# Kernel tuning notes

Hardware: AMD Instinct MI355X
Metric: run time of the kernel (lower is better)

## Reference

```python
import jax, jax.numpy as jnp
import numpy as np

BASE_TEMP = 0.07
CLASS_TEMPS = jnp.array([0.08, 0.05, 0.10], dtype=jnp.float32)  # idx 0,1,2
EPS = 1e-08


def setup_inputs() -> dict:
    key = jax.random.key(0)
    k1, k2 = jax.random.split(key)
    B, D = 8192, 128
    embeddings = jax.random.normal(k1, (B, D), dtype=jnp.float32)
    labels = jax.random.randint(k2, (B,), 0, 3, dtype=jnp.int64)
    return {"embeddings": embeddings, "labels": labels}


def reference(embeddings, labels):
    B = embeddings.shape[0]
    # per-row temperature from the row's class label
    temps = CLASS_TEMPS[labels]  # [B]
    sim = jnp.matmul(embeddings, embeddings.T)  # [B, B]
    logits = sim / temps[:, None]
    # subtract detached row max (stability, gradient-stopped as in .detach())
    logits = logits - jax.lax.stop_gradient(jnp.max(logits, axis=1, keepdims=True))
    # denominator includes the self term (original sums exp over all j)
    log_prob = logits - jnp.log(jnp.sum(jnp.exp(logits), axis=1, keepdims=True) + EPS)
    # positives: same label, excluding self
    pos_mask = (labels[:, None] == labels[None, :]).astype(jnp.float32)
    pos_mask = pos_mask * (1.0 - jnp.eye(B, dtype=jnp.float32))
    pos_count = jnp.sum(pos_mask, axis=1)  # [B]
    valid = pos_count > 0
    loss_i = -(BASE_TEMP / temps) * jnp.sum(pos_mask * log_prob, axis=1) / (pos_count + EPS)
    n_valid = jnp.sum(valid.astype(jnp.float32))
    total = jnp.sum(jnp.where(valid, loss_i, 0.0))
    return jnp.where(n_valid > 0, total / jnp.maximum(n_valid, 1.0), 0.0)
```

## Files before the change

kernel.cpp:

```cpp
#include <hip/hip_runtime.h>
#include <hip/hip_bf16.h>


#define B_ROWS 8192
#define D_DIM 128
#define BASE_TEMP 0.07f
#define LOG2E 1.4426950408889634f
#define LN2 0.6931471805599453f
#define FIX_SCALE 1048576.0f

typedef __bf16 bf16x8 __attribute__((ext_vector_type(8)));
typedef __bf16 bf16x4 __attribute__((ext_vector_type(4)));
typedef float floatx16 __attribute__((ext_vector_type(16)));
typedef unsigned long long u64;

__device__ __forceinline__ float class_invtemp(int lbl) {
    return (lbl == 0) ? 12.5f : ((lbl == 1) ? 20.0f : 10.0f);
}

__device__ __forceinline__ u64 fix64(float v) {
    return (u64)(long long)llrintf(v * FIX_SCALE);
}

__global__ __launch_bounds__(256) void kz_zero(u64* __restrict__ a) {
    a[threadIdx.x] = 0ull;
    a[256 + threadIdx.x] = 0ull;
}

__global__ __launch_bounds__(256) void k0_prep(
        const float* __restrict__ E, const int* __restrict__ labels,
        __bf16* __restrict__ Ebf, float* __restrict__ nrm,
        u64* __restrict__ Sfix , u64* __restrict__ cntfix ) {
    const int blk = blockIdx.x;
    const int tid = threadIdx.x;
    const int row0 = blk * 32;

    __shared__ float sh[3][128];
    __shared__ int scnt[3];
    if (tid < 3) scnt[tid] = 0;

    const float4* src = reinterpret_cast<const float4*>(E + (size_t)row0 * D_DIM);
    #pragma unroll
    for (int p = 0; p < 4; ++p) {
        int idx = p * 256 + tid;
        float4 v = src[idx];
        int r = idx >> 5, k4 = idx & 31;
        int R = row0 + r;
        int T = R >> 5;
        int l = (R & 31) + ((k4 >> 1) & 1) * 32;
        int c = k4 >> 2;
        size_t dst = (size_t)T * 4096 + c * 512 + l * 8 + (k4 & 1) * 4;
        bf16x4 o = { (__bf16)v.x, (__bf16)v.y, (__bf16)v.z, (__bf16)v.w };
        *reinterpret_cast<bf16x4*>(Ebf + dst) = o;
        float s = v.x * v.x + v.y * v.y + v.z * v.z + v.w * v.w;
        s += __shfl_xor(s, 1);  s += __shfl_xor(s, 2);  s += __shfl_xor(s, 4);
        s += __shfl_xor(s, 8);  s += __shfl_xor(s, 16);
        if ((tid & 31) == 0) nrm[R] = s;
    }

    const int d = tid & 127, half = tid >> 7;
    float s0 = 0.f, s1 = 0.f, s2 = 0.f;
    #pragma unroll 4
    for (int r2 = 0; r2 < 16; ++r2) {
        int r = row0 + half * 16 + r2;
        float v = E[(size_t)r * D_DIM + d];
        int l = labels[r];
        s0 += (l == 0) ? v : 0.f;
        s1 += (l == 1) ? v : 0.f;
        s2 += (l == 2) ? v : 0.f;
    }
    if (half == 1) { sh[0][d] = s0; sh[1][d] = s1; sh[2][d] = s2; }
    __syncthreads();
    if (half == 0) {
        atomicAdd(&Sfix[d],       fix64(s0 + sh[0][d]));
        atomicAdd(&Sfix[128 + d], fix64(s1 + sh[1][d]));
        atomicAdd(&Sfix[256 + d], fix64(s2 + sh[2][d]));
    }
    if (tid < 32) atomicAdd(&scnt[labels[row0 + tid]], 1);
    __syncthreads();
    if (tid < 3) atomicAdd(&cntfix[tid], (u64)scnt[tid]);
}

__global__ __launch_bounds__(256, 3) void k2_stats(
        const __bf16* __restrict__ Ebf, const int* __restrict__ labels,
        const float* __restrict__ nrm, float* __restrict__ part,
        int nsplit, int jrange) {
    const int lane = threadIdx.x & 63;
    const int wave = threadIdx.x >> 6;
    const int split = blockIdx.y;
    const int j0 = split * jrange;
    const int col = lane & 31;
    const int icol = blockIdx.x * 128 + wave * 32 + col;

    const float bscale = class_invtemp(labels[icol]) * LOG2E;
    const float negm = -bscale * nrm[icol];

    const int iT = blockIdx.x * 4 + wave;
    const __bf16* bbase = Ebf + (size_t)iT * 4096 + lane * 8;
    bf16x8 Bf[8];
    #pragma unroll
    for (int c = 0; c < 8; ++c) {
        bf16x8 raw = *reinterpret_cast<const bf16x8*>(bbase + c * 512);
        bf16x8 sc;
        #pragma unroll
        for (int e = 0; e < 8; ++e) sc[e] = (__bf16)((float)raw[e] * bscale);
        Bf[c] = sc;
    }

    const __bf16* abase = Ebf + ((size_t)(j0 >> 5)) * 4096 + lane * 8;
    bf16x8 A0[8], A1[8];
    #pragma unroll
    for (int c = 0; c < 8; ++c)
        A0[c] = *reinterpret_cast<const bf16x8*>(abase + c * 512);

    float Zacc[16];
    #pragma unroll
    for (int r = 0; r < 16; ++r) Zacc[r] = 0.f;
    const int nsteps = jrange >> 5;

    auto k2_step = [&](const bf16x8* Ab) {
        floatx16 acc;
        #pragma unroll
        for (int r = 0; r < 16; ++r) acc[r] = negm;
        #pragma unroll
        for (int c = 0; c < 8; ++c)
            acc = __builtin_amdgcn_mfma_f32_32x32x16_bf16(Ab[c], Bf[c], acc, 0, 0, 0);
        #pragma unroll
        for (int r = 0; r < 16; ++r)
            Zacc[r] += __builtin_amdgcn_exp2f(acc[r]);
    };

    for (int s = 0; s < nsteps; s += 2) {
        {
            const __bf16* ap = abase + (size_t)(s + 1) * 4096;
            #pragma unroll
            for (int c = 0; c < 8; ++c)
                A1[c] = *reinterpret_cast<const bf16x8*>(ap + c * 512);
            k2_step(A0);
        }
        {
            if (s + 2 < nsteps) {
                const __bf16* ap = abase + (size_t)(s + 2) * 4096;
                #pragma unroll
                for (int c = 0; c < 8; ++c)
                    A0[c] = *reinterpret_cast<const bf16x8*>(ap + c * 512);
            }
            k2_step(A1);
        }
    }

    float t0 = (Zacc[0] + Zacc[1]) + (Zacc[2] + Zacc[3]);
    float t1 = (Zacc[4] + Zacc[5]) + (Zacc[6] + Zacc[7]);
    float t2 = (Zacc[8] + Zacc[9]) + (Zacc[10] + Zacc[11]);
    float t3 = (Zacc[12] + Zacc[13]) + (Zacc[14] + Zacc[15]);
    float Zt = (t0 + t1) + (t2 + t3);
    Zt += __shfl_xor(Zt, 32);
    if (lane < 32)
        part[(size_t)split * B_ROWS + icol] = Zt;
}

__global__ __launch_bounds__(256) void k3_rowloss(
        const float* __restrict__ E, const int* __restrict__ labels,
        const u64* __restrict__ Sfix, const u64* __restrict__ cntfix,
        const float* __restrict__ nrm, const float* __restrict__ part,
        int nsplit, u64* __restrict__ lossfix, u64* __restrict__ validfix,
        unsigned int* __restrict__ done, float* __restrict__ out) {
    __shared__ float sS[384];
    const int tid = threadIdx.x;
    if (tid < 128) {
        sS[tid]       = (float)(long long)Sfix[tid]       * (1.0f / FIX_SCALE);
        sS[128 + tid] = (float)(long long)Sfix[128 + tid] * (1.0f / FIX_SCALE);
        sS[256 + tid] = (float)(long long)Sfix[256 + tid] * (1.0f / FIX_SCALE);
    }
    __syncthreads();

    const int r = tid >> 3, g = tid & 7;
    const int i = blockIdx.x * 32 + r;
    const int lab = labels[i];
    const float invt = class_invtemp(lab);

    const float4* er = reinterpret_cast<const float4*>(E + (size_t)i * D_DIM);
    const float4* sr = reinterpret_cast<const float4*>(&sS[lab * 128]);
    float dotS = 0.f;
    #pragma unroll
    for (int q = 0; q < 4; ++q) {
        float4 v = er[g * 4 + q];
        float4 s = sr[g * 4 + q];
        dotS += v.x * s.x + v.y * s.y + v.z * s.z + v.w * s.w;
    }
    float Zp = 0.f;
    for (int p = g; p < nsplit; p += 8)
        Zp += part[(size_t)p * B_ROWS + i];

    #pragma unroll
    for (int off = 1; off < 8; off <<= 1) {
        dotS += __shfl_xor(dotS, off);
        Zp   += __shfl_xor(Zp, off);
    }

    float loss = 0.f;
    int valid = 0;
    if (g == 0) {
        const float nr = nrm[i];
        const float C = (float)(long long)cntfix[lab] - 1.0f;
        const float lse = invt * nr + LN2 * __builtin_amdgcn_logf(Zp);
        const float P_nat = invt * (dotS - nr);
        if (C > 0.f) {
            loss = -(BASE_TEMP * invt) * (P_nat - C * lse) / (C + 1e-8f);
            valid = 1;
        }
    }
    loss  += __shfl_down(loss, 8);   valid += __shfl_down(valid, 8);
    loss  += __shfl_down(loss, 16);  valid += __shfl_down(valid, 16);
    loss  += __shfl_down(loss, 32);  valid += __shfl_down(valid, 32);

    __shared__ float rl[4];
    __shared__ int rv[4];
    if ((tid & 63) == 0) { rl[tid >> 6] = loss; rv[tid >> 6] = valid; }
    __syncthreads();
    if (tid == 0) {
        float bt = (rl[0] + rl[1]) + (rl[2] + rl[3]);
        int bv = (rv[0] + rv[1]) + (rv[2] + rv[3]);
        atomicAdd(lossfix, fix64(bt));
        atomicAdd(validfix, (u64)bv);
        __threadfence();
        unsigned int t = atomicAdd(done, 1u);
        if (t == gridDim.x - 1) {
            u64 L = atomicAdd(lossfix, 0ull);
            u64 V = atomicAdd(validfix, 0ull);
            double T = (double)(long long)L * (1.0 / (double)FIX_SCALE);
            double N = (double)(long long)V;
            out[0] = (N > 0.0) ? (float)(T / fmax(N, 1.0)) : 0.f;
        }
    }
}

extern "C" void kernel_launch(void* const* d_in, const int* in_sizes, int n_in,
                              void* d_out, int out_size, void* d_ws, size_t ws_size,
                              hipStream_t stream) {
    const float* E = (const float*)d_in[0];
    const int* labels = (const int*)d_in[1];
    float* out = (float*)d_out;
    char* ws = (char*)d_ws;

    const size_t OFF_EBF = 0;
    const size_t OFF_ATOM = (size_t)2 << 20;
    const size_t OFF_NRM = OFF_ATOM + 4096;
    const size_t OFF_PART = OFF_NRM + (size_t)B_ROWS * 4;

    int nsplit = 8;
    if (ws_size >= OFF_PART + (size_t)32 * B_ROWS * 4) nsplit = 32;
    else if (ws_size >= OFF_PART + (size_t)16 * B_ROWS * 4) nsplit = 16;
    const int jrange = B_ROWS / nsplit;

    __bf16* Ebf = (__bf16*)(ws + OFF_EBF);
    u64* Sfix = (u64*)(ws + OFF_ATOM);
    u64* cntfix = Sfix + 384;
    u64* lossfix = Sfix + 388;
    u64* validfix = Sfix + 389;
    unsigned int* done = (unsigned int*)(Sfix + 390);
    float* nrm = (float*)(ws + OFF_NRM);
    float* part = (float*)(ws + OFF_PART);

    kz_zero<<<1, 256, 0, stream>>>(Sfix);
    k0_prep<<<256, 256, 0, stream>>>(E, labels, Ebf, nrm, Sfix, cntfix);
    k2_stats<<<dim3(64, nsplit), 256, 0, stream>>>(Ebf, labels, nrm, part, nsplit, jrange);
    k3_rowloss<<<256, 256, 0, stream>>>(E, labels, Sfix, cntfix, nrm, part,
                                        nsplit, lossfix, validfix, done, out);
}
```

Baseline: 55.57 us.

## Fuse all stages into one cooperative persistent kernel with grid syncs

Replaces the four separate launches (zero, prep, stats, rowloss) with a single cooperative kernel that separates the phases with grid-wide syncs. Fixed-point atomics are replaced by per-block partial buffers that are reduced deterministically. The prep stage now also writes a pre-scaled bf16 copy, so the MFMA stage no longer rescales B. The MFMA chain is split into two independent accumulators to expose instruction-level parallelism. In exchange it pays grid-sync costs and may get lower occupancy from the larger fused kernel.

```diff
diff --git a/kernel.cpp b/kernel.cpp
--- a/kernel.cpp
+++ b/kernel.cpp
@@ -1,236 +1,259 @@
 #include <hip/hip_runtime.h>
 #include <hip/hip_bf16.h>
+#include <hip/hip_cooperative_groups.h>
+
+namespace cg = cooperative_groups;
 
 
 #define B_ROWS 8192
 #define D_DIM 128
+#define NSPLIT 32
+#define JRANGE (B_ROWS / NSPLIT)
+#define NSTEPS (JRANGE / 32)
+#define NUNITS (64 * NSPLIT)
 #define BASE_TEMP 0.07f
 #define LOG2E 1.4426950408889634f
 #define LN2 0.6931471805599453f
-#define FIX_SCALE 1048576.0f
 
 typedef __bf16 bf16x8 __attribute__((ext_vector_type(8)));
 typedef __bf16 bf16x4 __attribute__((ext_vector_type(4)));
 typedef float floatx16 __attribute__((ext_vector_type(16)));
-typedef unsigned long long u64;
 
 __device__ __forceinline__ float class_invtemp(int lbl) {
     return (lbl == 0) ? 12.5f : ((lbl == 1) ? 20.0f : 10.0f);
 }
 
-__device__ __forceinline__ u64 fix64(float v) {
-    return (u64)(long long)llrintf(v * FIX_SCALE);
-}
-
-__global__ __launch_bounds__(256) void kz_zero(u64* __restrict__ a) {
-    a[threadIdx.x] = 0ull;
-    a[256 + threadIdx.x] = 0ull;
-}
-
-__global__ __launch_bounds__(256) void k0_prep(
+__global__ __launch_bounds__(256, 3) void supcon_all(
         const float* __restrict__ E, const int* __restrict__ labels,
-        __bf16* __restrict__ Ebf, float* __restrict__ nrm,
-        u64* __restrict__ Sfix , u64* __restrict__ cntfix ) {
-    const int blk = blockIdx.x;
+        __bf16* __restrict__ Ebf, __bf16* __restrict__ Ebs,
+        float* __restrict__ nrm,
+        float* __restrict__ Spart ,
+        int* __restrict__ cntpart ,
+        float* __restrict__ S , float* __restrict__ counts ,
+        float* __restrict__ part ,
+        float* __restrict__ bpart , float* __restrict__ out) {
+    cg::grid_group gg = cg::this_grid();
     const int tid = threadIdx.x;
-    const int row0 = blk * 32;
+    const int bid = blockIdx.x;
+    const int nblk = gridDim.x;
 
     __shared__ float sh[3][128];
     __shared__ int scnt[3];
-    if (tid < 3) scnt[tid] = 0;
-
-    const float4* src = reinterpret_cast<const float4*>(E + (size_t)row0 * D_DIM);
-    #pragma unroll
-    for (int p = 0; p < 4; ++p) {
-        int idx = p * 256 + tid;
-        float4 v = src[idx];
-        int r = idx >> 5, k4 = idx & 31;
-        int R = row0 + r;
-        int T = R >> 5;
-        int l = (R & 31) + ((k4 >> 1) & 1) * 32;
-        int c = k4 >> 2;
-        size_t dst = (size_t)T * 4096 + c * 512 + l * 8 + (k4 & 1) * 4;
-        bf16x4 o = { (__bf16)v.x, (__bf16)v.y, (__bf16)v.z, (__bf16)v.w };
-        *reinterpret_cast<bf16x4*>(Ebf + dst) = o;
-        float s = v.x * v.x + v.y * v.y + v.z * v.z + v.w * v.w;
-        s += __shfl_xor(s, 1);  s += __shfl_xor(s, 2);  s += __shfl_xor(s, 4);
-        s += __shfl_xor(s, 8);  s += __shfl_xor(s, 16);
-        if ((tid & 31) == 0) nrm[R] = s;
-    }
-
-    const int d = tid & 127, half = tid >> 7;
-    float s0 = 0.f, s1 = 0.f, s2 = 0.f;
-    #pragma unroll 4
-    for (int r2 = 0; r2 < 16; ++r2) {
-        int r = row0 + half * 16 + r2;
-        float v = E[(size_t)r * D_DIM + d];
-        int l = labels[r];
-        s0 += (l == 0) ? v : 0.f;
-        s1 += (l == 1) ? v : 0.f;
-        s2 += (l == 2) ? v : 0.f;
-    }
-    if (half == 1) { sh[0][d] = s0; sh[1][d] = s1; sh[2][d] = s2; }
-    __syncthreads();
-    if (half == 0) {
-        atomicAdd(&Sfix[d],       fix64(s0 + sh[0][d]));
-        atomicAdd(&Sfix[128 + d], fix64(s1 + sh[1][d]));
-        atomicAdd(&Sfix[256 + d], fix64(s2 + sh[2][d]));
-    }
-    if (tid < 32) atomicAdd(&scnt[labels[row0 + tid]], 1);
-    __syncthreads();
-    if (tid < 3) atomicAdd(&cntfix[tid], (u64)scnt[tid]);
-}
-
-__global__ __launch_bounds__(256, 3) void k2_stats(
-        const __bf16* __restrict__ Ebf, const int* __restrict__ labels,
-        const float* __restrict__ nrm, float* __restrict__ part,
-        int nsplit, int jrange) {
-    const int lane = threadIdx.x & 63;
-    const int wave = threadIdx.x >> 6;
-    const int split = blockIdx.y;
-    const int j0 = split * jrange;
-    const int col = lane & 31;
-    const int icol = blockIdx.x * 128 + wave * 32 + col;
-
-    const float bscale = class_invtemp(labels[icol]) * LOG2E;
-    const float negm = -bscale * nrm[icol];
-
-    const int iT = blockIdx.x * 4 + wave;
-    const __bf16* bbase = Ebf + (size_t)iT * 4096 + lane * 8;
-    bf16x8 Bf[8];
-    #pragma unroll
-    for (int c = 0; c < 8; ++c) {
-        bf16x8 raw = *reinterpret_cast<const bf16x8*>(bbase + c * 512);
-        bf16x8 sc;
-        #pragma unroll
-        for (int e = 0; e < 8; ++e) sc[e] = (__bf16)((float)raw[e] * bscale);
-        Bf[c] = sc;
-    }
-
-    const __bf16* abase = Ebf + ((size_t)(j0 >> 5)) * 4096 + lane * 8;
-    bf16x8 A0[8], A1[8];
-    #pragma unroll
-    for (int c = 0; c < 8; ++c)
-        A0[c] = *reinterpret_cast<const bf16x8*>(abase + c * 512);
-
-    float Zacc[16];
-    #pragma unroll
-    for (int r = 0; r < 16; ++r) Zacc[r] = 0.f;
-    const int nsteps = jrange >> 5;
-
-    auto k2_step = [&](const bf16x8* Ab) {
-        floatx16 acc;
-        #pragma unroll
-        for (int r = 0; r < 16; ++r) acc[r] = negm;
+    __shared__ float rl[4];
+    __shared__ int rv[4];
+
+    for (int g = bid; g < 256; g += nblk) {
+        const int row0 = g * 32;
+        if (tid < 3) scnt[tid] = 0;
+        __syncthreads();
+        const float4* src = reinterpret_cast<const float4*>(E + (size_t)row0 * D_DIM);
+        #pragma unroll
+        for (int p = 0; p < 4; ++p) {
+            int idx = p * 256 + tid;
+            float4 v = src[idx];
+            int r = idx >> 5, k4 = idx & 31;
+            int R = row0 + r;
+            float sc = class_invtemp(labels[R]) * LOG2E;
+            int T = R >> 5;
+            int l = (R & 31) + ((k4 >> 1) & 1) * 32;
+            int c = k4 >> 2;
+            size_t dst = (size_t)T * 4096 + c * 512 + l * 8 + (k4 & 1) * 4;
+            bf16x4 o  = { (__bf16)v.x, (__bf16)v.y, (__bf16)v.z, (__bf16)v.w };
+            bf16x4 os = { (__bf16)(v.x * sc), (__bf16)(v.y * sc),
+                          (__bf16)(v.z * sc), (__bf16)(v.w * sc) };
+            *reinterpret_cast<bf16x4*>(Ebf + dst) = o;
+            *reinterpret_cast<bf16x4*>(Ebs + dst) = os;
+            float s = v.x * v.x + v.y * v.y + v.z * v.z + v.w * v.w;
+            s += __shfl_xor(s, 1);  s += __shfl_xor(s, 2);  s += __shfl_xor(s, 4);
+            s += __shfl_xor(s, 8);  s += __shfl_xor(s, 16);
+            if ((tid & 31) == 0) nrm[R] = s;
+        }
+        const int d = tid & 127, half = tid >> 7;
+        float s0 = 0.f, s1 = 0.f, s2 = 0.f;
+        #pragma unroll 4
+        for (int r2 = 0; r2 < 16; ++r2) {
+            int r = row0 + half * 16 + r2;
+            float v = E[(size_t)r * D_DIM + d];
+            int l = labels[r];
+            s0 += (l == 0) ? v : 0.f;
+            s1 += (l == 1) ? v : 0.f;
+            s2 += (l == 2) ? v : 0.f;
+        }
+        if (half == 1) { sh[0][d] = s0; sh[1][d] = s1; sh[2][d] = s2; }
+        if (tid < 32) atomicAdd(&scnt[labels[row0 + tid]], 1);
+        __syncthreads();
+        if (half == 0) {
+            Spart[((size_t)g * 3 + 0) * 128 + d] = s0 + sh[0][d];
+            Spart[((size_t)g * 3 + 1) * 128 + d] = s1 + sh[1][d];
+            Spart[((size_t)g * 3 + 2) * 128 + d] = s2 + sh[2][d];
+        }
+        if (tid < 3) cntpart[g * 4 + tid] = scnt[tid];
+        __syncthreads();
+    }
+    gg.sync();
+
+    if (bid < 3) {
+        if (tid < 128) {
+            float a = 0.f;
+            #pragma unroll 8
+            for (int g = 0; g < 256; ++g)
+                a += Spart[((size_t)g * 3 + bid) * 128 + tid];
+            S[bid * 128 + tid] = a;
+        }
+    } else if (bid == 3 && tid < 3) {
+        int a = 0;
+        #pragma unroll 8
+        for (int g = 0; g < 256; ++g) a += cntpart[g * 4 + tid];
+        counts[tid] = (float)a;
+    }
+
+    for (int u = bid; u < NUNITS; u += nblk) {
+        const int itile = u >> 5;
+        const int split = u & 31;
+        const int j0 = split * JRANGE;
+        const int lane = tid & 63;
+        const int wave = tid >> 6;
+        const int col = lane & 31;
+        const int icol = itile * 128 + wave * 32 + col;
+
+        const float bscale = class_invtemp(labels[icol]) * LOG2E;
+        const float negm = -bscale * nrm[icol];
+
+        const int iT = itile * 4 + wave;
+        const __bf16* bbase = Ebs + (size_t)iT * 4096 + lane * 8;
+        bf16x8 Bf[8];
         #pragma unroll
         for (int c = 0; c < 8; ++c)
-            acc = __builtin_amdgcn_mfma_f32_32x32x16_bf16(Ab[c], Bf[c], acc, 0, 0, 0);
-        #pragma unroll
-        for (int r = 0; r < 16; ++r)
-            Zacc[r] += __builtin_amdgcn_exp2f(acc[r]);
-    };
-
-    for (int s = 0; s < nsteps; s += 2) {
-        {
-            const __bf16* ap = abase + (size_t)(s + 1) * 4096;
+            Bf[c] = *reinterpret_cast<const bf16x8*>(bbase + c * 512);
+
+        const __bf16* abase = Ebf + ((size_t)(j0 >> 5)) * 4096 + lane * 8;
+        bf16x8 A0[8], A1[8];
+        #pragma unroll
+        for (int c = 0; c < 8; ++c)
+            A0[c] = *reinterpret_cast<const bf16x8*>(abase + c * 512);
+
+        float Zacc[8];
+        #pragma unroll
+        for (int r = 0; r < 8; ++r) Zacc[r] = 0.f;
+
+        auto k2_step = [&](const bf16x8* Ab) {
+            floatx16 a0, a1;
             #pragma unroll
-            for (int c = 0; c < 8; ++c)
-                A1[c] = *reinterpret_cast<const bf16x8*>(ap + c * 512);
-            k2_step(A0);
-        }
-        {
-            if (s + 2 < nsteps) {
-                const __bf16* ap = abase + (size_t)(s + 2) * 4096;
+            for (int r = 0; r < 16; ++r) { a0[r] = negm; a1[r] = 0.f; }
+            a0 = __builtin_amdgcn_mfma_f32_32x32x16_bf16(Ab[0], Bf[0], a0, 0, 0, 0);
+            a1 = __builtin_amdgcn_mfma_f32_32x32x16_bf16(Ab[4], Bf[4], a1, 0, 0, 0);
+            a0 = __builtin_amdgcn_mfma_f32_32x32x16_bf16(Ab[1], Bf[1], a0, 0, 0, 0);
+            a1 = __builtin_amdgcn_mfma_f32_32x32x16_bf16(Ab[5], Bf[5], a1, 0, 0, 0);
+            a0 = __builtin_amdgcn_mfma_f32_32x32x16_bf16(Ab[2], Bf[2], a0, 0, 0, 0);
+            a1 = __builtin_amdgcn_mfma_f32_32x32x16_bf16(Ab[6], Bf[6], a1, 0, 0, 0);
+            a0 = __builtin_amdgcn_mfma_f32_32x32x16_bf16(Ab[3], Bf[3], a0, 0, 0, 0);
+            a1 = __builtin_amdgcn_mfma_f32_32x32x16_bf16(Ab[7], Bf[7], a1, 0, 0, 0);
+            #pragma unroll
+            for (int r8 = 0; r8 < 8; ++r8) {
+                float z = __builtin_amdgcn_exp2f(a0[2 * r8] + a1[2 * r8])
+                        + __builtin_amdgcn_exp2f(a0[2 * r8 + 1] + a1[2 * r8 + 1]);
+                Zacc[r8] += z;
+            }
+        };
+
+        for (int s = 0; s < NSTEPS; s += 2) {
+            {
+                const __bf16* ap = abase + (size_t)(s + 1) * 4096;
                 #pragma unroll
                 for (int c = 0; c < 8; ++c)
-                    A0[c] = *reinterpret_cast<const bf16x8*>(ap + c * 512);
+                    A1[c] = *reinterpret_cast<const bf16x8*>(ap + c * 512);
+                k2_step(A0);
             }
-            k2_step(A1);
-        }
-    }
-
-    float t0 = (Zacc[0] + Zacc[1]) + (Zacc[2] + Zacc[3]);
-    float t1 = (Zacc[4] + Zacc[5]) + (Zacc[6] + Zacc[7]);
-    float t2 = (Zacc[8] + Zacc[9]) + (Zacc[10] + Zacc[11]);
-    float t3 = (Zacc[12] + Zacc[13]) + (Zacc[14] + Zacc[15]);
-    float Zt = (t0 + t1) + (t2 + t3);
-    Zt += __shfl_xor(Zt, 32);
-    if (lane < 32)
-        part[(size_t)split * B_ROWS + icol] = Zt;
-}
-
-__global__ __launch_bounds__(256) void k3_rowloss(
-        const float* __restrict__ E, const int* __restrict__ labels,
-        const u64* __restrict__ Sfix, const u64* __restrict__ cntfix,
-        const float* __restrict__ nrm, const float* __restrict__ part,
-        int nsplit, u64* __restrict__ lossfix, u64* __restrict__ validfix,
-        unsigned int* __restrict__ done, float* __restrict__ out) {
-    __shared__ float sS[384];
-    const int tid = threadIdx.x;
+            {
+                if (s + 2 < NSTEPS) {
+                    const __bf16* ap = abase + (size_t)(s + 2) * 4096;
+                    #pragma unroll
+                    for (int c = 0; c < 8; ++c)
+                        A0[c] = *reinterpret_cast<const bf16x8*>(ap + c * 512);
+                }
+                k2_step(A1);
+            }
+        }
+
+        float t0 = (Zacc[0] + Zacc[1]) + (Zacc[2] + Zacc[3]);
+        float t1 = (Zacc[4] + Zacc[5]) + (Zacc[6] + Zacc[7]);
+        float Zt = t0 + t1;
+        Zt += __shfl_xor(Zt, 32);
+        if (lane < 32)
+            part[(size_t)split * B_ROWS + icol] = Zt;
+    }
+    gg.sync();
+
     if (tid < 128) {
-        sS[tid]       = (float)(long long)Sfix[tid]       * (1.0f / FIX_SCALE);
-        sS[128 + tid] = (float)(long long)Sfix[128 + tid] * (1.0f / FIX_SCALE);
-        sS[256 + tid] = (float)(long long)Sfix[256 + tid] * (1.0f / FIX_SCALE);
+        sh[0][tid] = S[tid];
+        sh[1][tid] = S[128 + tid];
+        sh[2][tid] = S[256 + tid];
     }
     __syncthreads();
-
-    const int r = tid >> 3, g = tid & 7;
-    const int i = blockIdx.x * 32 + r;
-    const int lab = labels[i];
-    const float invt = class_invtemp(lab);
-
-    const float4* er = reinterpret_cast<const float4*>(E + (size_t)i * D_DIM);
-    const float4* sr = reinterpret_cast<const float4*>(&sS[lab * 128]);
-    float dotS = 0.f;
-    #pragma unroll
-    for (int q = 0; q < 4; ++q) {
-        float4 v = er[g * 4 + q];
-        float4 s = sr[g * 4 + q];
-        dotS += v.x * s.x + v.y * s.y + v.z * s.z + v.w * s.w;
-    }
-    float Zp = 0.f;
-    for (int p = g; p < nsplit; p += 8)
-        Zp += part[(size_t)p * B_ROWS + i];
-
-    #pragma unroll
-    for (int off = 1; off < 8; off <<= 1) {
-        dotS += __shfl_xor(dotS, off);
-        Zp   += __shfl_xor(Zp, off);
-    }
-
-    float loss = 0.f;
-    int valid = 0;
-    if (g == 0) {
-        const float nr = nrm[i];
-        const float C = (float)(long long)cntfix[lab] - 1.0f;
-        const float lse = invt * nr + LN2 * __builtin_amdgcn_logf(Zp);
-        const float P_nat = invt * (dotS - nr);
-        if (C > 0.f) {
-            loss = -(BASE_TEMP * invt) * (P_nat - C * lse) / (C + 1e-8f);
-            valid = 1;
-        }
-    }
-    loss  += __shfl_down(loss, 8);   valid += __shfl_down(valid, 8);
-    loss  += __shfl_down(loss, 16);  valid += __shfl_down(valid, 16);
-    loss  += __shfl_down(loss, 32);  valid += __shfl_down(valid, 32);
-
-    __shared__ float rl[4];
-    __shared__ int rv[4];
-    if ((tid & 63) == 0) { rl[tid >> 6] = loss; rv[tid >> 6] = valid; }
-    __syncthreads();
-    if (tid == 0) {
-        float bt = (rl[0] + rl[1]) + (rl[2] + rl[3]);
-        int bv = (rv[0] + rv[1]) + (rv[2] + rv[3]);
-        atomicAdd(lossfix, fix64(bt));
-        atomicAdd(validfix, (u64)bv);
-        __threadfence();
-        unsigned int t = atomicAdd(done, 1u);
-        if (t == gridDim.x - 1) {
-            u64 L = atomicAdd(lossfix, 0ull);
-            u64 V = atomicAdd(validfix, 0ull);
-            double T = (double)(long long)L * (1.0 / (double)FIX_SCALE);
-            double N = (double)(long long)V;
-            out[0] = (N > 0.0) ? (float)(T / fmax(N, 1.0)) : 0.f;
+    for (int v = bid; v < 256; v += nblk) {
+        const int r = tid >> 3, g = tid & 7;
+        const int i = v * 32 + r;
+        const int lab = labels[i];
+        const float invt = class_invtemp(lab);
+
+        const float4* er = reinterpret_cast<const float4*>(E + (size_t)i * D_DIM);
+        const float4* sr = reinterpret_cast<const float4*>(&sh[lab][0]);
+        float dotS = 0.f;
+        #pragma unroll
+        for (int q = 0; q < 4; ++q) {
+            float4 vv = er[g * 4 + q];
+            float4 ss = sr[g * 4 + q];
+            dotS += vv.x * ss.x + vv.y * ss.y + vv.z * ss.z + vv.w * ss.w;
+        }
+        float Zp = 0.f;
+        #pragma unroll
+        for (int p = 0; p < NSPLIT / 8; ++p)
+            Zp += part[(size_t)(g + p * 8) * B_ROWS + i];
+
+        #pragma unroll
+        for (int off = 1; off < 8; off <<= 1) {
+            dotS += __shfl_xor(dotS, off);
+            Zp   += __shfl_xor(Zp, off);
+        }
+
+        float loss = 0.f;
+        int valid = 0;
+        if (g == 0) {
+            const float nr = nrm[i];
+            const float C = counts[lab] - 1.0f;
+            const float lse = invt * nr + LN2 * __builtin_amdgcn_logf(Zp);
+            const float P_nat = invt * (dotS - nr);
+            if (C > 0.f) {
+                loss = -(BASE_TEMP * invt) * (P_nat - C * lse) / (C + 1e-8f);
+                valid = 1;
+            }
+        }
+        loss += __shfl_down(loss, 8);   valid += __shfl_down(valid, 8);
+        loss += __shfl_down(loss, 16);  valid += __shfl_down(valid, 16);
+        loss += __shfl_down(loss, 32);  valid += __shfl_down(valid, 32);
+        if ((tid & 63) == 0) { rl[tid >> 6] = loss; rv[tid >> 6] = valid; }
+        __syncthreads();
+        if (tid == 0) {
+            bpart[v * 2 + 0] = (rl[0] + rl[1]) + (rl[2] + rl[3]);
+            bpart[v * 2 + 1] = (float)((rv[0] + rv[1]) + (rv[2] + rv[3]));
+        }
+        __syncthreads();
+    }
+    gg.sync();
+
+    if (bid == 0) {
+        float T = bpart[tid * 2], N = bpart[tid * 2 + 1];
+        #pragma unroll
+        for (int off = 32; off; off >>= 1) {
+            T += __shfl_down(T, off);
+            N += __shfl_down(N, off);
+        }
+        if ((tid & 63) == 0) { rl[tid >> 6] = T; rv[tid >> 6] = (int)N; }
+        __syncthreads();
+        if (tid == 0) {
+            float Tt = (rl[0] + rl[1]) + (rl[2] + rl[3]);
+            float Nt = (float)((rv[0] + rv[1]) + (rv[2] + rv[3]));
+            out[0] = (Nt > 0.f) ? Tt / fmaxf(Nt, 1.f) : 0.f;
         }
     }
 }
@@ -243,28 +266,38 @@
     float* out = (float*)d_out;
     char* ws = (char*)d_ws;
 
-    const size_t OFF_EBF = 0;
-    const size_t OFF_ATOM = (size_t)2 << 20;
-    const size_t OFF_NRM = OFF_ATOM + 4096;
-    const size_t OFF_PART = OFF_NRM + (size_t)B_ROWS * 4;
-
-    int nsplit = 8;
-    if (ws_size >= OFF_PART + (size_t)32 * B_ROWS * 4) nsplit = 32;
-    else if (ws_size >= OFF_PART + (size_t)16 * B_ROWS * 4) nsplit = 16;
-    const int jrange = B_ROWS / nsplit;
-
+    const size_t OFF_EBF   = 0;
+    const size_t OFF_EBS   = (size_t)2 << 20;
+    const size_t OFF_NRM   = (size_t)4 << 20;
+    const size_t OFF_SPART = OFF_NRM + 32768;
+    const size_t OFF_CNTP  = OFF_SPART + 393216;
+    const size_t OFF_S     = OFF_CNTP + 4096;
+    const size_t OFF_CNT   = OFF_S + 2048;
+    const size_t OFF_BPART = OFF_CNT + 64;
+    const size_t OFF_PART  = (size_t)5 << 20;
+
+    const float* Ec = E;
+    const int* lc = labels;
     __bf16* Ebf = (__bf16*)(ws + OFF_EBF);
-    u64* Sfix = (u64*)(ws + OFF_ATOM);
-    u64* cntfix = Sfix + 384;
-    u64* lossfix = Sfix + 388;
-    u64* validfix = Sfix + 389;
-    unsigned int* done = (unsigned int*)(Sfix + 390);
+    __bf16* Ebs = (__bf16*)(ws + OFF_EBS);
     float* nrm = (float*)(ws + OFF_NRM);
+    float* Spart = (float*)(ws + OFF_SPART);
+    int* cntpart = (int*)(ws + OFF_CNTP);
+    float* S = (float*)(ws + OFF_S);
+    float* counts = (float*)(ws + OFF_CNT);
+    float* bpart = (float*)(ws + OFF_BPART);
     float* part = (float*)(ws + OFF_PART);
 
-    kz_zero<<<1, 256, 0, stream>>>(Sfix);
-    k0_prep<<<256, 256, 0, stream>>>(E, labels, Ebf, nrm, Sfix, cntfix);
-    k2_stats<<<dim3(64, nsplit), 256, 0, stream>>>(Ebf, labels, nrm, part, nsplit, jrange);
-    k3_rowloss<<<256, 256, 0, stream>>>(E, labels, Sfix, cntfix, nrm, part,
-                                        nsplit, lossfix, validfix, done, out);
+    int occ = 0;
+    if (hipOccupancyMaxActiveBlocksPerMultiprocessor(
+            &occ, (const void*)supcon_all, 256, 0) != hipSuccess || occ < 1)
+        occ = 1;
+    if (occ > 3) occ = 3;
+    dim3 grid(256 * occ);
+
+    void* args[] = { (void*)&Ec, (void*)&lc, (void*)&Ebf, (void*)&Ebs,
+                     (void*)&nrm, (void*)&Spart, (void*)&cntpart, (void*)&S,
+                     (void*)&counts, (void*)&part, (void*)&bpart, (void*)&out };
+    hipLaunchCooperativeKernel((const void*)supcon_all, grid, dim3(256),
+                               args, 0, stream);
 }
```

New measurement: 142.2 us. 2.56x slower.
